# Optimization experiments

Hardware: AMD Instinct MI355X
Metric: run time of the kernel (lower is better)

The kernel has to match this reference:

```python
import jax, jax.numpy as jnp
import numpy as np

S, N, NSUB, F, HID, NH = 8, 20000, 4000, 128, 64, 8


def setup_inputs() -> dict:
    key = jax.random.key(0)
    ks = jax.random.split(key, 24)
    # unique sorted node indices per snapshot (matches snap.nodes used for gather + scatter-pad)
    nodes = jnp.stack([jnp.sort(jax.random.permutation(ks[i], N)[:NSUB]) for i in range(S)])
    # dense normalized adjacency proxy (norm_adj.to_dense()); scaled so rows sum ~1
    adj = jax.random.uniform(ks[8], (S, NSUB, NSUB), dtype=jnp.float32) * (2.0 / NSUB)
    p = lambda k, shp: jax.random.normal(k, shp, dtype=jnp.float32) * 0.02
    return {
        "nodes": nodes,
        "adj": adj,
        "emb": p(ks[9], (N, F)),
        "W1": p(ks[10], (F, HID)), "b1": jnp.zeros((HID,), jnp.float32),
        "W2": p(ks[11], (HID, HID)), "b2": jnp.zeros((HID,), jnp.float32),
        "time_emb": p(ks[12], (2 * S - 1, NH)),
        "Wq": p(ks[13], (HID, HID)), "bq": jnp.zeros((HID,), jnp.float32),
        "Wk": p(ks[14], (HID, HID)), "bk": jnp.zeros((HID,), jnp.float32),
        "Wv": p(ks[15], (HID, HID)), "bv": jnp.zeros((HID,), jnp.float32),
        "Wo": p(ks[16], (HID, HID)), "bo": jnp.zeros((HID,), jnp.float32),
    }


def reference(nodes, adj, emb, W1, b1, W2, b2, time_emb,
              Wq, bq, Wk, bk, Wv, bv, Wo, bo):
    s, nsub = nodes.shape
    n_total, _ = emb.shape
    hid = W1.shape[1]
    nh = time_emb.shape[1]
    dh = hid // nh
    # per-snapshot GCN encode (2 layers of A @ (X W) + b, ReLU), vectorized over snapshots
    feat = emb[nodes]                                            # [S, n, F]
    h = jax.nn.relu(jnp.einsum('sij,sjh->sih', adj, feat @ W1) + b1)
    h = jax.nn.relu(jnp.einsum('sij,sjh->sih', adj, h @ W2) + b2)
    # scatter-pad into zero buffer of size nodes_num (output[pos_idx] = x)
    x = jnp.zeros((s, n_total, hid), h.dtype).at[jnp.arange(s)[:, None], nodes].set(h)
    x = x.transpose(1, 0, 2)                                     # [N, S, HID]
    # relative-position time bias: Embedding(2S-1, NH)[rel_matrix] -> [NH, S, S]
    rel = jnp.arange(s)[None, :] - jnp.arange(s)[:, None] + s - 1
    bias = time_emb[rel].transpose(2, 0, 1)
    # multi-head attention over the snapshot axis, batch = nodes
    q = (x @ Wq + bq).reshape(n_total, s, nh, dh) * (dh ** -0.5)
    k = (x @ Wk + bk).reshape(n_total, s, nh, dh)
    v = (x @ Wv + bv).reshape(n_total, s, nh, dh)
    scores = jnp.einsum('nqhd,nkhd->nhqk', q, k) + bias          # [N, NH, S, S]
    attn = jax.nn.softmax(scores, axis=-1)
    o = jnp.einsum('nhqk,nkhd->nqhd', attn, v).reshape(n_total, s, hid)
    o = o @ Wo + bo
    o = o.transpose(1, 0, 2)                                     # [S, N, HID]
    # gather active nodes back, then structure decoder z @ z.T per snapshot
    z = jnp.take_along_axis(o, nodes[:, :, None], axis=1)        # [S, n, HID]
    out = jnp.einsum('sid,sjd->sij', z, z)                       # [S, n, n]
    return out
```

## Files before the change

### kernel.cpp

```cpp
#include <hip/hip_runtime.h>
#include <hip/hip_bf16.h>
#include <cstdint>

#define S 8
#define NTOT 20000
#define NSUB 4000
#define F 128
#define HID 64
#define NH 8
#define DH 8
#define KSPL 2016

typedef __attribute__((ext_vector_type(8))) short bf16x8;
typedef __attribute__((ext_vector_type(4))) short bf16x4;
typedef __attribute__((ext_vector_type(4))) float f32x4;

__device__ __forceinline__ short f2bf(float f) {
  union { __hip_bfloat16 h; short s; } u;
  u.h = __float2bfloat16(f);
  return u.s;
}

__device__ __forceinline__ void gload16(const void* gsrc, void* ldst) {
  __builtin_amdgcn_global_load_lds(
      (const __attribute__((address_space(1))) void*)gsrc,
      (__attribute__((address_space(3))) void*)ldst, 16, 0, 0);
}

__global__ void k_pos_init(int* __restrict__ posIdx) {
  int t = blockIdx.x * 256 + threadIdx.x;
  if (t < NTOT * S) posIdx[t] = -1;
}

__global__ void k_pos_scatter(const int* __restrict__ nodes, int* __restrict__ posIdx) {
  int t = blockIdx.x * 256 + threadIdx.x;
  if (t < S * NSUB) {
    int s = t / NSUB, i = t - s * NSUB;
    posIdx[nodes[t] * S + s] = i;
  }
}

__global__ __launch_bounds__(256) void k_feat_w1(const int* __restrict__ nodes,
                                                 const float* __restrict__ emb,
                                                 const float* __restrict__ W1,
                                                 short* __restrict__ Pt) {
  __shared__ __align__(16) float feat[16][F];
  __shared__ float tr[64][17];
  int t = threadIdx.x;
  int s = blockIdx.x / 250;
  int i0 = (blockIdx.x - s * 250) * 16;
  int gr0 = blockIdx.x * 16;
  int lr = t >> 4, lc = (t & 15) * 8;
  int n = nodes[gr0 + lr];
  *(f32x4*)&feat[lr][lc]     = *(const f32x4*)(emb + (size_t)n * F + lc);
  *(f32x4*)&feat[lr][lc + 4] = *(const f32x4*)(emb + (size_t)n * F + lc + 4);
  __syncthreads();
  int j = t & 63, ig = t >> 6;
  float acc[4] = {0.f, 0.f, 0.f, 0.f};
  for (int k = 0; k < F; ++k) {
    float w = W1[k * HID + j];
    #pragma unroll
    for (int i = 0; i < 4; ++i) acc[i] += feat[ig * 4 + i][k] * w;
  }
  #pragma unroll
  for (int i = 0; i < 4; ++i) tr[j][ig * 4 + i] = acc[i];
  __syncthreads();
  int jr = t >> 2, seg = (t & 3) * 4;
  bf16x4 o;
  #pragma unroll
  for (int u = 0; u < 4; ++u) o[u] = f2bf(tr[jr][seg + u]);
  *(bf16x4*)(Pt + ((size_t)s * HID + jr) * NSUB + i0 + seg) = o;
}

__global__ __launch_bounds__(256) void k_adj(const float* __restrict__ adj,
                                             const short* __restrict__ Pt,
                                             float* __restrict__ part) {
  __shared__ __align__(16) float As[2][64 * 32];
  __shared__ __align__(16) short Bs[2][64 * 32];
  int bid = blockIdx.x;
  int s = bid & 7;
  int rest = bid >> 3;
  int z = rest & 1, mb = rest >> 1;
  int ks_ = z ? KSPL : 0, ke_ = z ? NSUB : KSPL;
  int tid = threadIdx.x;
  int w = tid >> 6, lane = tid & 63, l15 = lane & 15, g = lane >> 4;
  int m0 = mb * 64;
  const float* adjS = adj + (size_t)s * NSUB * NSUB;
  const short* PtS  = Pt  + (size_t)s * HID * NSUB;

  int arow0 = tid >> 3;
  int aslot = tid & 7;
  int r0g = m0 + arow0;        r0g = r0g < NSUB ? r0g : NSUB - 1;
  int r1g = m0 + 32 + arow0;   r1g = r1g < NSUB ? r1g : NSUB - 1;
  int c0 = aslot ^ (arow0 & 7);
  int c1 = aslot ^ ((32 + arow0) & 7);
  const float* asrc0 = adjS + (size_t)r0g * NSUB + c0 * 4;
  const float* asrc1 = adjS + (size_t)r1g * NSUB + c1 * 4;
  int bcol  = tid >> 2;
  int bchunk = (tid & 3) ^ (bcol & 3);
  const short* bsrc0 = PtS + (size_t)bcol * NSUB + bchunk * 8;

  char* As0 = (char*)&As[0][0];
  char* Bs0 = (char*)&Bs[0][0];
  int wb = w * 1024;

  int arow = w * 16 + l15;
  int fa0 = arow * 128 + (((g * 2)     ^ (arow & 7)) * 16);
  int fa1 = arow * 128 + (((g * 2 + 1) ^ (arow & 7)) * 16);
  int fb[4];
  #pragma unroll
  for (int nf = 0; nf < 4; ++nf) {
    int col = nf * 16 + l15;
    fb[nf] = col * 64 + ((g ^ (col & 3)) * 16);
  }

  f32x4 acc[4];
  #pragma unroll
  for (int nf = 0; nf < 4; ++nf) acc[nf] = (f32x4){0.f, 0.f, 0.f, 0.f};

  gload16(asrc0 + ks_, As0 + 0    + wb);
  gload16(asrc1 + ks_, As0 + 4096 + wb);
  gload16(bsrc0 + ks_, Bs0 + wb);

  int nsteps = (ke_ - ks_) >> 5;
  for (int t = 0; t < nsteps; ++t) {
    __syncthreads();
    int cur = t & 1;
    if (t + 1 < nsteps) {
      int kn = ks_ + (t + 1) * 32;
      int nb  = (cur ^ 1) * 8192;
      int nbs = (cur ^ 1) * 4096;
      gload16(asrc0 + kn, As0 + nb + 0    + wb);
      gload16(asrc1 + kn, As0 + nb + 4096 + wb);
      gload16(bsrc0 + kn, Bs0 + nbs + wb);
    }
    const char* Ab = As0 + cur * 8192;
    const char* Bb = Bs0 + cur * 4096;
    f32x4 a0 = *(const f32x4*)(Ab + fa0);
    f32x4 a1 = *(const f32x4*)(Ab + fa1);
    bf16x8 afr;
    afr[0] = f2bf(a0.x); afr[1] = f2bf(a0.y); afr[2] = f2bf(a0.z); afr[3] = f2bf(a0.w);
    afr[4] = f2bf(a1.x); afr[5] = f2bf(a1.y); afr[6] = f2bf(a1.z); afr[7] = f2bf(a1.w);
    bf16x8 b0 = *(const bf16x8*)(Bb + fb[0]);
    bf16x8 b1 = *(const bf16x8*)(Bb + fb[1]);
    bf16x8 b2 = *(const bf16x8*)(Bb + fb[2]);
    bf16x8 b3 = *(const bf16x8*)(Bb + fb[3]);
    acc[0] = __builtin_amdgcn_mfma_f32_16x16x32_bf16(afr, b0, acc[0], 0, 0, 0);
    acc[1] = __builtin_amdgcn_mfma_f32_16x16x32_bf16(afr, b1, acc[1], 0, 0, 0);
    acc[2] = __builtin_amdgcn_mfma_f32_16x16x32_bf16(afr, b2, acc[2], 0, 0, 0);
    acc[3] = __builtin_amdgcn_mfma_f32_16x16x32_bf16(afr, b3, acc[3], 0, 0, 0);
  }

  float* P = part + (size_t)(z * S + s) * NSUB * HID;
  #pragma unroll
  for (int nf = 0; nf < 4; ++nf) {
    int col = nf * 16 + l15;
    #pragma unroll
    for (int r = 0; r < 4; ++r) {
      int row = m0 + w * 16 + g * 4 + r;
      if (row < NSUB) P[(size_t)row * HID + col] = acc[nf][r];
    }
  }
}

__global__ __launch_bounds__(256) void k_reduce1(const float* __restrict__ part,
                                                 const float* __restrict__ b1,
                                                 const float* __restrict__ W2,
                                                 short* __restrict__ Pt2) {
  __shared__ float h[32][65];
  int bid = blockIdx.x;
  int s = bid / 125, i0 = (bid - s * 125) * 32;
  int t = threadIdx.x;
  int r = t >> 3, c8 = (t & 7) * 8;
  const size_t zs = (size_t)S * NSUB * HID;
  const float* P0 = part + ((size_t)s * NSUB + i0 + r) * HID + c8;
  #pragma unroll
  for (int u = 0; u < 8; ++u)
    h[r][c8 + u] = fmaxf(P0[u] + P0[zs + u] + b1[c8 + u], 0.f);
  __syncthreads();
  int j = t & 63, ib = t >> 6;
  float acc[8];
  #pragma unroll
  for (int u = 0; u < 8; ++u) acc[u] = 0.f;
  for (int k = 0; k < HID; ++k) {
    float w = W2[k * HID + j];
    #pragma unroll
    for (int u = 0; u < 8; ++u) acc[u] += h[ib * 8 + u][k] * w;
  }
  bf16x8 o;
  #pragma unroll
  for (int u = 0; u < 8; ++u) o[u] = f2bf(acc[u]);
  *(bf16x8*)(Pt2 + ((size_t)s * HID + j) * NSUB + i0 + ib * 8) = o;
}

__global__ __launch_bounds__(256) void k_reduce2(const float* __restrict__ part,
                                                 const float* __restrict__ b2,
                                                 float* __restrict__ H) {
  size_t idx = ((size_t)blockIdx.x * 256 + threadIdx.x) * 8;
  const size_t zs = (size_t)S * NSUB * HID;
  const float* P0 = part + idx;
  int c = (int)(idx & 63);
  f32x4 r0, r1;
  #pragma unroll
  for (int u = 0; u < 4; ++u) {
    r0[u] = fmaxf(P0[u]     + P0[zs + u]     + b2[c + u], 0.f);
    r1[u] = fmaxf(P0[4 + u] + P0[zs + 4 + u] + b2[c + 4 + u], 0.f);
  }
  *(f32x4*)(H + idx) = r0;
  *(f32x4*)(H + idx + 4) = r1;
}

__global__ __launch_bounds__(256) void k_attn(const float* __restrict__ H,
                                              const int* __restrict__ posIdx,
                                              const float* __restrict__ Wq, const float* __restrict__ bq,
                                              const float* __restrict__ Wk, const float* __restrict__ bk,
                                              const float* __restrict__ Wv, const float* __restrict__ bv,
                                              const float* __restrict__ Wo, const float* __restrict__ bo,
                                              const float* __restrict__ te,
                                              short* __restrict__ Zb) {
  __shared__ __align__(16) float xk[4][S][HID];
  __shared__ __align__(16) float qs[4][S][HID];
  __shared__ __align__(16) float ks[4][S][HID];
  __shared__ __align__(16) float vs[4][S][HID];
  __shared__ __align__(16) float os[4][S][HID];
  int w = threadIdx.x >> 6;
  int lane = threadIdx.x & 63;
  int n = blockIdx.x * 4 + w;
  int pi[S];
  #pragma unroll
  for (int s = 0; s < S; ++s) {
    pi[s] = posIdx[n * S + s];
    xk[w][s][lane] = (pi[s] >= 0) ? H[((size_t)s * NSUB + pi[s]) * HID + lane] : 0.f;
  }
  __syncthreads();
  float aq[S], ak[S], av[S];
  #pragma unroll
  for (int s = 0; s < S; ++s) { aq[s] = bq[lane]; ak[s] = bk[lane]; av[s] = bv[lane]; }
  for (int k = 0; k < HID; ++k) {
    float wq = Wq[k*HID + lane], wk_ = Wk[k*HID + lane], wv = Wv[k*HID + lane];
    #pragma unroll
    for (int s = 0; s < S; ++s) {
      float xv = xk[w][s][k];
      aq[s] += xv * wq; ak[s] += xv * wk_; av[s] += xv * wv;
    }
  }
  const float qscale = 0.35355339059327373f;
  #pragma unroll
  for (int s = 0; s < S; ++s) {
    qs[w][s][lane] = aq[s] * qscale;
    ks[w][s][lane] = ak[s];
    vs[w][s][lane] = av[s];
  }
  __syncthreads();
  int h = lane >> 3, sq = lane & 7;
  f32x4 q0 = *(const f32x4*)&qs[w][sq][h * DH];
  f32x4 q1 = *(const f32x4*)&qs[w][sq][h * DH + 4];
  float sc[S];
  #pragma unroll
  for (int t = 0; t < S; ++t) {
    f32x4 k0v = *(const f32x4*)&ks[w][t][h * DH];
    f32x4 k1v = *(const f32x4*)&ks[w][t][h * DH + 4];
    float d = q0.x*k0v.x + q0.y*k0v.y + q0.z*k0v.z + q0.w*k0v.w
            + q1.x*k1v.x + q1.y*k1v.y + q1.z*k1v.z + q1.w*k1v.w;
    sc[t] = d + te[(t - sq + S - 1) * NH + h];
  }
  float m = sc[0];
  #pragma unroll
  for (int t = 1; t < S; ++t) m = fmaxf(m, sc[t]);
  float sum = 0.f;
  #pragma unroll
  for (int t = 0; t < S; ++t) { sc[t] = expf(sc[t] - m); sum += sc[t]; }
  float inv = 1.f / sum;
  f32x4 o0 = (f32x4){0.f,0.f,0.f,0.f}, o1 = (f32x4){0.f,0.f,0.f,0.f};
  #pragma unroll
  for (int t = 0; t < S; ++t) {
    f32x4 v0 = *(const f32x4*)&vs[w][t][h * DH];
    f32x4 v1 = *(const f32x4*)&vs[w][t][h * DH + 4];
    #pragma unroll
    for (int u = 0; u < 4; ++u) { o0[u] += sc[t] * v0[u]; o1[u] += sc[t] * v1[u]; }
  }
  #pragma unroll
  for (int u = 0; u < 4; ++u) { o0[u] *= inv; o1[u] *= inv; }
  *(f32x4*)&os[w][sq][h * DH]     = o0;
  *(f32x4*)&os[w][sq][h * DH + 4] = o1;
  __syncthreads();
  float ao[S];
  #pragma unroll
  for (int s = 0; s < S; ++s) ao[s] = bo[lane];
  for (int k = 0; k < HID; ++k) {
    float wo = Wo[k*HID + lane];
    #pragma unroll
    for (int s = 0; s < S; ++s) ao[s] += os[w][s][k] * wo;
  }
  #pragma unroll
  for (int s = 0; s < S; ++s)
    if (pi[s] >= 0) Zb[((size_t)s * NSUB + pi[s]) * HID + lane] = f2bf(ao[s]);
}

__global__ __launch_bounds__(256) void k_dec(const short* __restrict__ Zb,
                                             float* __restrict__ out) {
  __shared__ __align__(16) float tr[4][16][68];
  int bid = blockIdx.x;
  int s = bid & 7;
  int tt = bid >> 3;
  int by = tt / 63, bx = tt - by * 63;
  int wave = threadIdx.x >> 6, lane = threadIdx.x & 63;
  int l15 = lane & 15, g = lane >> 4;
  int m0 = by * 64 + wave * 16;
  int n0 = bx * 64;
  const short* ZS = Zb + (size_t)s * NSUB * HID;
  int mrow = m0 + l15;
  int mc = mrow < NSUB ? mrow : NSUB - 1;
  bf16x8 a0 = *(const bf16x8*)(ZS + (size_t)mc * HID + g * 8);
  bf16x8 a1 = *(const bf16x8*)(ZS + (size_t)mc * HID + 32 + g * 8);
  f32x4 acc[4];
  #pragma unroll
  for (int nf = 0; nf < 4; ++nf) acc[nf] = (f32x4){0.f, 0.f, 0.f, 0.f};
  #pragma unroll
  for (int nf = 0; nf < 4; ++nf) {
    int ncol = n0 + nf * 16 + l15;
    int nc = ncol < NSUB ? ncol : NSUB - 1;
    bf16x8 b0 = *(const bf16x8*)(ZS + (size_t)nc * HID + g * 8);
    bf16x8 b1 = *(const bf16x8*)(ZS + (size_t)nc * HID + 32 + g * 8);
    acc[nf] = __builtin_amdgcn_mfma_f32_16x16x32_bf16(a0, b0, acc[nf], 0, 0, 0);
    acc[nf] = __builtin_amdgcn_mfma_f32_16x16x32_bf16(a1, b1, acc[nf], 0, 0, 0);
  }
  #pragma unroll
  for (int nf = 0; nf < 4; ++nf)
    #pragma unroll
    for (int r = 0; r < 4; ++r)
      tr[wave][g * 4 + r][nf * 16 + l15] = acc[nf][r];
  __syncthreads();
  float* outS = out + (size_t)s * NSUB * NSUB;
  #pragma unroll
  for (int p = 0; p < 4; ++p) {
    int rr = p * 4 + g;
    int grow = m0 + rr;
    int gcol = n0 + l15 * 4;
    f32x4 v = *(const f32x4*)&tr[wave][rr][l15 * 4];
    if (grow < NSUB && gcol < NSUB)
      __builtin_nontemporal_store(v, (f32x4*)(outS + (size_t)grow * NSUB + gcol));
  }
}

extern "C" void kernel_launch(void* const* d_in, const int* in_sizes, int n_in,
                              void* d_out, int out_size, void* d_ws, size_t ws_size,
                              hipStream_t stream) {
  const int*   nodes = (const int*)d_in[0];
  const float* adj   = (const float*)d_in[1];
  const float* emb   = (const float*)d_in[2];
  const float* W1    = (const float*)d_in[3];
  const float* b1    = (const float*)d_in[4];
  const float* W2    = (const float*)d_in[5];
  const float* b2    = (const float*)d_in[6];
  const float* te    = (const float*)d_in[7];
  const float* Wq    = (const float*)d_in[8];
  const float* bq    = (const float*)d_in[9];
  const float* Wk    = (const float*)d_in[10];
  const float* bk    = (const float*)d_in[11];
  const float* Wv    = (const float*)d_in[12];
  const float* bv    = (const float*)d_in[13];
  const float* Wo    = (const float*)d_in[14];
  const float* bo    = (const float*)d_in[15];
  float* outp = (float*)d_out;

  float* part = (float*)d_ws;
  float* H    = part + 2 * (size_t)S * NSUB * HID;
  short* Pt   = (short*)(H + (size_t)S * NSUB * HID);
  short* Zb   = Pt + (size_t)S * HID * NSUB;
  int* posIdx = (int*)(Zb + (size_t)S * NSUB * HID);

  k_pos_init<<<(NTOT*S + 255)/256, 256, 0, stream>>>(posIdx);
  k_pos_scatter<<<(S*NSUB + 255)/256, 256, 0, stream>>>(nodes, posIdx);

  k_feat_w1<<<2000, 256, 0, stream>>>(nodes, emb, W1, Pt);
  k_adj<<<1008, 256, 0, stream>>>(adj, Pt, part);
  k_reduce1<<<1000, 256, 0, stream>>>(part, b1, W2, Pt);
  k_adj<<<1008, 256, 0, stream>>>(adj, Pt, part);
  k_reduce2<<<1000, 256, 0, stream>>>(part, b2, H);
  k_attn<<<NTOT/4, 256, 0, stream>>>(H, posIdx, Wq, bq, Wk, bk, Wv, bv, Wo, bo, te, Zb);
  k_dec<<<63*63*8, 256, 0, stream>>>(Zb, outp);
}
```

Baseline: 505.5 us.

## Drop split-K in adjacency GEMM, use 64-wide K tiles and fuse bias-ReLU epilogue

Removes the two-way split-K of the adjacency GEMM, so each block now walks the full K range in 64-wide steps with padded Pt rows (NSUBP) and out-of-range adj columns redirected to a valid address. The second layer's bias+ReLU moves into the GEMM epilogue, which removes the k_reduce2 pass and the partial-sum buffers. This cuts partial-sum traffic and one kernel launch. The cost is half as many blocks (504) and double the LDS per block, which lowers parallelism and occupancy.

New measurement: 485.4 us. -4.0%, faster.

```diff
diff --git a/kernel.cpp b/kernel.cpp
--- a/kernel.cpp
+++ b/kernel.cpp
@@ -5,11 +5,12 @@
 #define S 8
 #define NTOT 20000
 #define NSUB 4000
+#define NSUBP 4032
+#define NST 63
 #define F 128
 #define HID 64
 #define NH 8
 #define DH 8
-#define KSPL 2016
 
 typedef __attribute__((ext_vector_type(8))) short bf16x8;
 typedef __attribute__((ext_vector_type(4))) short bf16x4;
@@ -38,6 +39,13 @@
     int s = t / NSUB, i = t - s * NSUB;
     posIdx[nodes[t] * S + s] = i;
   }
+}
+
+__global__ void k_pt_pad(short* __restrict__ Pt) {
+  int t = blockIdx.x * 256 + threadIdx.x;
+  int seg = t >> 2, off = (t & 3) * 8;
+  bf16x8 z = (bf16x8){0,0,0,0,0,0,0,0};
+  *(bf16x8*)(Pt + (size_t)seg * NSUBP + NSUB + off) = z;
 }
 
 __global__ __launch_bounds__(256) void k_feat_w1(const int* __restrict__ nodes,
@@ -69,96 +77,116 @@
   bf16x4 o;
   #pragma unroll
   for (int u = 0; u < 4; ++u) o[u] = f2bf(tr[jr][seg + u]);
-  *(bf16x4*)(Pt + ((size_t)s * HID + jr) * NSUB + i0 + seg) = o;
-}
-
+  *(bf16x4*)(Pt + ((size_t)s * HID + jr) * NSUBP + i0 + seg) = o;
+}
+
+template<int MODE>
 __global__ __launch_bounds__(256) void k_adj(const float* __restrict__ adj,
                                              const short* __restrict__ Pt,
-                                             float* __restrict__ part) {
-  __shared__ __align__(16) float As[2][64 * 32];
-  __shared__ __align__(16) short Bs[2][64 * 32];
+                                             const float* __restrict__ bias,
+                                             float* __restrict__ out) {
+  __shared__ __align__(16) float As[2][64 * 64];
+  __shared__ __align__(16) short Bs[2][64 * 64];
   int bid = blockIdx.x;
   int s = bid & 7;
-  int rest = bid >> 3;
-  int z = rest & 1, mb = rest >> 1;
-  int ks_ = z ? KSPL : 0, ke_ = z ? NSUB : KSPL;
+  int mb = bid >> 3;
   int tid = threadIdx.x;
   int w = tid >> 6, lane = tid & 63, l15 = lane & 15, g = lane >> 4;
   int m0 = mb * 64;
   const float* adjS = adj + (size_t)s * NSUB * NSUB;
-  const short* PtS  = Pt  + (size_t)s * HID * NSUB;
-
-  int arow0 = tid >> 3;
-  int aslot = tid & 7;
-  int r0g = m0 + arow0;        r0g = r0g < NSUB ? r0g : NSUB - 1;
-  int r1g = m0 + 32 + arow0;   r1g = r1g < NSUB ? r1g : NSUB - 1;
-  int c0 = aslot ^ (arow0 & 7);
-  int c1 = aslot ^ ((32 + arow0) & 7);
-  const float* asrc0 = adjS + (size_t)r0g * NSUB + c0 * 4;
-  const float* asrc1 = adjS + (size_t)r1g * NSUB + c1 * 4;
-  int bcol  = tid >> 2;
-  int bchunk = (tid & 3) ^ (bcol & 3);
-  const short* bsrc0 = PtS + (size_t)bcol * NSUB + bchunk * 8;
+  const short* PtS  = Pt  + (size_t)s * HID * NSUBP;
+
+  int rbase = w * 4 + (lane >> 4);
+  int sigA = l15;
+  int clogA = (sigA & 8) | ((sigA & 7) ^ (rbase & 7));
+  int acolf = clogA * 4;
+  const float* arow[4];
+  #pragma unroll
+  for (int p = 0; p < 4; ++p) {
+    int rg = m0 + p * 16 + rbase;
+    rg = rg < NSUB ? rg : NSUB - 1;
+    arow[p] = adjS + (size_t)rg * NSUB;
+  }
+  int sigB = lane & 7;
+  int clogB = sigB ^ ((lane >> 3) & 7);
+  const short* bsrc[2];
+  #pragma unroll
+  for (int p = 0; p < 2; ++p) {
+    int col = p * 32 + w * 8 + (lane >> 3);
+    bsrc[p] = PtS + (size_t)col * NSUBP + clogB * 8;
+  }
 
   char* As0 = (char*)&As[0][0];
   char* Bs0 = (char*)&Bs[0][0];
   int wb = w * 1024;
 
-  int arow = w * 16 + l15;
-  int fa0 = arow * 128 + (((g * 2)     ^ (arow & 7)) * 16);
-  int fa1 = arow * 128 + (((g * 2 + 1) ^ (arow & 7)) * 16);
-  int fb[4];
+  int arowf = w * 16 + l15;
+  int aoff = arowf * 256 + (((2 * g) ^ (arowf & 7)) * 16);
+  int boff[4];
   #pragma unroll
   for (int nf = 0; nf < 4; ++nf) {
     int col = nf * 16 + l15;
-    fb[nf] = col * 64 + ((g ^ (col & 3)) * 16);
+    boff[nf] = col * 128 + ((g ^ (col & 7)) * 16);
   }
 
   f32x4 acc[4];
   #pragma unroll
   for (int nf = 0; nf < 4; ++nf) acc[nf] = (f32x4){0.f, 0.f, 0.f, 0.f};
 
-  gload16(asrc0 + ks_, As0 + 0    + wb);
-  gload16(asrc1 + ks_, As0 + 4096 + wb);
-  gload16(bsrc0 + ks_, Bs0 + wb);
-
-  int nsteps = (ke_ - ks_) >> 5;
-  for (int t = 0; t < nsteps; ++t) {
+  #pragma unroll
+  for (int p = 0; p < 4; ++p)
+    gload16(arow[p] + acolf, As0 + p * 4096 + wb);
+  #pragma unroll
+  for (int p = 0; p < 2; ++p)
+    gload16(bsrc[p], Bs0 + p * 4096 + wb);
+
+  for (int t = 0; t < NST; ++t) {
     __syncthreads();
     int cur = t & 1;
-    if (t + 1 < nsteps) {
-      int kn = ks_ + (t + 1) * 32;
-      int nb  = (cur ^ 1) * 8192;
-      int nbs = (cur ^ 1) * 4096;
-      gload16(asrc0 + kn, As0 + nb + 0    + wb);
-      gload16(asrc1 + kn, As0 + nb + 4096 + wb);
-      gload16(bsrc0 + kn, Bs0 + nbs + wb);
+    if (t + 1 < NST) {
+      int kn = (t + 1) * 64;
+      bool ok = (kn + acolf) < NSUB;
+      const char* nA = As0 + (cur ^ 1) * 16384;
+      const char* nB = Bs0 + (cur ^ 1) * 8192;
+      #pragma unroll
+      for (int p = 0; p < 4; ++p)
+        gload16(ok ? (arow[p] + kn + acolf) : arow[p], (void*)(nA + p * 4096 + wb));
+      #pragma unroll
+      for (int p = 0; p < 2; ++p)
+        gload16(bsrc[p] + kn, (void*)(nB + p * 4096 + wb));
     }
-    const char* Ab = As0 + cur * 8192;
-    const char* Bb = Bs0 + cur * 4096;
-    f32x4 a0 = *(const f32x4*)(Ab + fa0);
-    f32x4 a1 = *(const f32x4*)(Ab + fa1);
-    bf16x8 afr;
-    afr[0] = f2bf(a0.x); afr[1] = f2bf(a0.y); afr[2] = f2bf(a0.z); afr[3] = f2bf(a0.w);
-    afr[4] = f2bf(a1.x); afr[5] = f2bf(a1.y); afr[6] = f2bf(a1.z); afr[7] = f2bf(a1.w);
-    bf16x8 b0 = *(const bf16x8*)(Bb + fb[0]);
-    bf16x8 b1 = *(const bf16x8*)(Bb + fb[1]);
-    bf16x8 b2 = *(const bf16x8*)(Bb + fb[2]);
-    bf16x8 b3 = *(const bf16x8*)(Bb + fb[3]);
-    acc[0] = __builtin_amdgcn_mfma_f32_16x16x32_bf16(afr, b0, acc[0], 0, 0, 0);
-    acc[1] = __builtin_amdgcn_mfma_f32_16x16x32_bf16(afr, b1, acc[1], 0, 0, 0);
-    acc[2] = __builtin_amdgcn_mfma_f32_16x16x32_bf16(afr, b2, acc[2], 0, 0, 0);
-    acc[3] = __builtin_amdgcn_mfma_f32_16x16x32_bf16(afr, b3, acc[3], 0, 0, 0);
-  }
-
-  float* P = part + (size_t)(z * S + s) * NSUB * HID;
+    const char* Ab = As0 + cur * 16384;
+    const char* Bb = Bs0 + cur * 8192;
+    f32x4 a0 = *(const f32x4*)(Ab + aoff);
+    f32x4 a1 = *(const f32x4*)(Ab + (aoff ^ 16));
+    f32x4 a2 = *(const f32x4*)(Ab + 128 + aoff);
+    f32x4 a3 = *(const f32x4*)(Ab + 128 + (aoff ^ 16));
+    bf16x8 af0, af1;
+    af0[0] = f2bf(a0.x); af0[1] = f2bf(a0.y); af0[2] = f2bf(a0.z); af0[3] = f2bf(a0.w);
+    af0[4] = f2bf(a1.x); af0[5] = f2bf(a1.y); af0[6] = f2bf(a1.z); af0[7] = f2bf(a1.w);
+    af1[0] = f2bf(a2.x); af1[1] = f2bf(a2.y); af1[2] = f2bf(a2.z); af1[3] = f2bf(a2.w);
+    af1[4] = f2bf(a3.x); af1[5] = f2bf(a3.y); af1[6] = f2bf(a3.z); af1[7] = f2bf(a3.w);
+    #pragma unroll
+    for (int nf = 0; nf < 4; ++nf) {
+      bf16x8 b0 = *(const bf16x8*)(Bb + boff[nf]);
+      bf16x8 b1 = *(const bf16x8*)(Bb + (boff[nf] ^ 64));
+      acc[nf] = __builtin_amdgcn_mfma_f32_16x16x32_bf16(af0, b0, acc[nf], 0, 0, 0);
+      acc[nf] = __builtin_amdgcn_mfma_f32_16x16x32_bf16(af1, b1, acc[nf], 0, 0, 0);
+    }
+  }
+
+  float* P = out + (size_t)s * NSUB * HID;
   #pragma unroll
   for (int nf = 0; nf < 4; ++nf) {
     int col = nf * 16 + l15;
+    float bv = (MODE == 1) ? bias[col] : 0.f;
     #pragma unroll
     for (int r = 0; r < 4; ++r) {
       int row = m0 + w * 16 + g * 4 + r;
-      if (row < NSUB) P[(size_t)row * HID + col] = acc[nf][r];
+      if (row < NSUB) {
+        if (MODE == 1) P[(size_t)row * HID + col] = fmaxf(acc[nf][r] + bv, 0.f);
+        else           P[(size_t)row * HID + col] = acc[nf][r];
+      }
     }
   }
 }
@@ -172,11 +200,10 @@
   int s = bid / 125, i0 = (bid - s * 125) * 32;
   int t = threadIdx.x;
   int r = t >> 3, c8 = (t & 7) * 8;
-  const size_t zs = (size_t)S * NSUB * HID;
   const float* P0 = part + ((size_t)s * NSUB + i0 + r) * HID + c8;
   #pragma unroll
   for (int u = 0; u < 8; ++u)
-    h[r][c8 + u] = fmaxf(P0[u] + P0[zs + u] + b1[c8 + u], 0.f);
+    h[r][c8 + u] = fmaxf(P0[u] + b1[c8 + u], 0.f);
   __syncthreads();
   int j = t & 63, ib = t >> 6;
   float acc[8];
@@ -190,24 +217,7 @@
   bf16x8 o;
   #pragma unroll
   for (int u = 0; u < 8; ++u) o[u] = f2bf(acc[u]);
-  *(bf16x8*)(Pt2 + ((size_t)s * HID + j) * NSUB + i0 + ib * 8) = o;
-}
-
-__global__ __launch_bounds__(256) void k_reduce2(const float* __restrict__ part,
-                                                 const float* __restrict__ b2,
-                                                 float* __restrict__ H) {
-  size_t idx = ((size_t)blockIdx.x * 256 + threadIdx.x) * 8;
-  const size_t zs = (size_t)S * NSUB * HID;
-  const float* P0 = part + idx;
-  int c = (int)(idx & 63);
-  f32x4 r0, r1;
-  #pragma unroll
-  for (int u = 0; u < 4; ++u) {
-    r0[u] = fmaxf(P0[u]     + P0[zs + u]     + b2[c + u], 0.f);
-    r1[u] = fmaxf(P0[4 + u] + P0[zs + 4 + u] + b2[c + 4 + u], 0.f);
-  }
-  *(f32x4*)(H + idx) = r0;
-  *(f32x4*)(H + idx + 4) = r1;
+  *(bf16x8*)(Pt2 + ((size_t)s * HID + j) * NSUBP + i0 + ib * 8) = o;
 }
 
 __global__ __launch_bounds__(256) void k_attn(const float* __restrict__ H,
@@ -365,19 +375,19 @@
   float* outp = (float*)d_out;
 
   float* part = (float*)d_ws;
-  float* H    = part + 2 * (size_t)S * NSUB * HID;
+  float* H    = part + (size_t)S * NSUB * HID;
   short* Pt   = (short*)(H + (size_t)S * NSUB * HID);
-  short* Zb   = Pt + (size_t)S * HID * NSUB;
+  short* Zb   = Pt + (size_t)S * HID * NSUBP;
   int* posIdx = (int*)(Zb + (size_t)S * NSUB * HID);
 
   k_pos_init<<<(NTOT*S + 255)/256, 256, 0, stream>>>(posIdx);
   k_pos_scatter<<<(S*NSUB + 255)/256, 256, 0, stream>>>(nodes, posIdx);
+  k_pt_pad<<<8, 256, 0, stream>>>(Pt);
 
   k_feat_w1<<<2000, 256, 0, stream>>>(nodes, emb, W1, Pt);
-  k_adj<<<1008, 256, 0, stream>>>(adj, Pt, part);
+  k_adj<0><<<504, 256, 0, stream>>>(adj, Pt, b1, part);
   k_reduce1<<<1000, 256, 0, stream>>>(part, b1, W2, Pt);
-  k_adj<<<1008, 256, 0, stream>>>(adj, Pt, part);
-  k_reduce2<<<1000, 256, 0, stream>>>(part, b2, H);
+  k_adj<1><<<504, 256, 0, stream>>>(adj, Pt, b2, H);
   k_attn<<<NTOT/4, 256, 0, stream>>>(H, posIdx, Wq, bq, Wk, bk, Wv, bv, Wo, bo, te, Zb);
   k_dec<<<63*63*8, 256, 0, stream>>>(Zb, outp);
 }
```
